# Performance work log

Measured on AMD Instinct MI355X. Metric: run time of the kernel, lower is better.

The kernel has to match this reference:

```python
import jax, jax.numpy as jnp
import numpy as np

B, N, H = 8, 128, 768      # batch, words, BERT hidden
HID, L = 384, 100          # MLP hidden, label_num


def setup_inputs() -> dict:
    key = jax.random.key(0)
    k0, k1, k2 = jax.random.split(key, 3)
    s = 0.02
    return {
        "repr_w": jax.random.normal(k0, (B, N, H), jnp.float32),
        "W1": jax.random.normal(k1, (2 * H, HID), jnp.float32) * s,
        "b1": jnp.zeros((HID,), jnp.float32),
        "W2": jax.random.normal(k2, (HID, L), jnp.float32) * s,
        "b2": jnp.zeros((L,), jnp.float32),
    }


def reference(repr_w, W1, b1, W2, b2):
    # Original: table[b,i,j] = concat(repr_w[b,j] (row_h), repr_w[b,i] (column_h))
    # then MLP: relu(table @ W1 + b1) @ W2 + b2  (dropout inactive in eval).
    # Decompose the concat-GEMM: concat(r_j, r_i) @ W1 == r_j @ W1[:H] + r_i @ W1[H:].
    W1_row, W1_col = W1[:H], W1[H:]
    p = jnp.einsum('bnh,hd->bnd', repr_w, W1_row)  # contribution indexed by j
    q = jnp.einsum('bnh,hd->bnd', repr_w, W1_col)  # contribution indexed by i
    h = jax.nn.relu(p[:, None, :, :] + q[:, :, None, :] + b1)  # [B,N,N,HID]
    return jnp.einsum('bijd,dl->bijl', h, W2) + b2              # [B,N,N,L]
```

## Files before the change

### kernel.cpp

```cpp
#include <hip/hip_runtime.h>
#include <hip/hip_bf16.h>

#define B_   8
#define N_   128
#define H_   768
#define HID_ 384
#define L_   100

typedef float f32x4 __attribute__((ext_vector_type(4)));
typedef short s16x8 __attribute__((ext_vector_type(8)));

__device__ __forceinline__ short f2bf(float f) {
    __hip_bfloat16 h = __float2bfloat16(f);
    return __builtin_bit_cast(short, h);
}

__device__ __forceinline__ void gl_lds16(const void* g, void* l) {
    __builtin_amdgcn_global_load_lds(
        (const __attribute__((address_space(1))) unsigned int*)g,
        (__attribute__((address_space(3))) unsigned int*)l, 16, 0, 0);
}

__global__ void prep_w1f(const float* __restrict__ W1, short* __restrict__ W1f) {
    int tid = blockIdx.x * 256 + threadIdx.x;
    if (tid >= 48 * 24 * 64) return;
    int lane = tid & 63;
    int kk   = (tid >> 6) % 24;
    int ct   = tid / (24 * 64);
    int c    = ct * 16 + (lane & 15);
    int k0   = kk * 32 + ((lane >> 4) << 3);
    short v[8];
#pragma unroll
    for (int e = 0; e < 8; ++e) {
        int k = k0 + e;
        float f = (c < HID_) ? W1[(size_t)k * HID_ + c]
                             : W1[(size_t)(H_ + k) * HID_ + (c - HID_)];
        v[e] = f2bf(f);
    }
    ((s16x8*)W1f)[tid] = *(const s16x8*)v;
}

__global__ void prep_w2f(const float* __restrict__ W2, short* __restrict__ W2f) {
    int tid = blockIdx.x * 256 + threadIdx.x;
    if (tid >= 12 * 7 * 64) return;
    int lane = tid & 63;
    int t    = (tid >> 6) % 7;
    int kk   = tid / (7 * 64);
    int c    = t * 16 + (lane & 15);
    int k0   = kk * 32 + ((lane >> 4) << 3);
    short v[8];
#pragma unroll
    for (int e = 0; e < 8; ++e) {
        float f = (c < L_) ? W2[(size_t)(k0 + e) * L_ + c] : 0.0f;
        v[e] = f2bf(f);
    }
    ((s16x8*)W2f)[tid] = *(const s16x8*)v;
}

__global__ __launch_bounds__(256) void pq_gemm(
    const float* __restrict__ repr, const short* __restrict__ W1f,
    const float* __restrict__ b1,
    float* __restrict__ Pt, float* __restrict__ Q)
{
    __shared__ float atile[192 * 16 * 4];
    const int rt   = blockIdx.x / 12;
    const int cg   = blockIdx.x % 12;
    const int w    = threadIdx.x >> 6;
    const int lane = threadIdx.x & 63;
    const int l15  = lane & 15;
    const int g    = lane >> 4;
    const int ct   = cg * 4 + w;
    const int row_g0 = rt * 16;

#pragma unroll
    for (int c = 0; c < 12; ++c) {
        int call = w * 12 + c;
        const float* src = repr + (size_t)(row_g0 + (lane & 15)) * H_
                         + (call * 4 + (lane >> 4)) * 4;
        gl_lds16(src, (char*)atile + call * 1024);
    }
    __syncthreads();

    f32x4 acc;
    acc[0] = 0.f; acc[1] = 0.f; acc[2] = 0.f; acc[3] = 0.f;
    const s16x8* bbase = (const s16x8*)W1f + (size_t)(ct * 24) * 64 + lane;

#pragma unroll 4
    for (int kk = 0; kk < 24; ++kk) {
        const int u0 = kk * 8 + g * 2;
        float a[8];
        *(float4*)&a[0] = *(const float4*)&atile[(u0 * 16 + l15) * 4];
        *(float4*)&a[4] = *(const float4*)&atile[((u0 + 1) * 16 + l15) * 4];
        s16x8 af;
#pragma unroll
        for (int e = 0; e < 8; ++e) af[e] = f2bf(a[e]);
        s16x8 bf = bbase[(size_t)kk * 64];
        acc = __builtin_amdgcn_mfma_f32_16x16x32_bf16(af, bf, acc, 0, 0, 0);
    }

    const int b = rt >> 3;
    const int c = ct * 16 + l15;
#pragma unroll
    for (int r = 0; r < 4; ++r) {
        int brow = (rt & 7) * 16 + g * 4 + r;
        float v = acc[r];
        if (c < HID_) {
            int slice = c >> 5, un = (c & 31) >> 2, e4 = c & 3;
            Pt[((((size_t)b * 12 + slice) * 8 + un) * 128 + brow) * 4 + e4] = v + b1[c];
        } else {
            Q[(size_t)(b * N_ + brow) * HID_ + (c - HID_)] = v;
        }
    }
}

__global__ __launch_bounds__(512, 4) void fused_out(
    const float* __restrict__ Pt, const float* __restrict__ Q,
    const short* __restrict__ W2f, const float* __restrict__ b2,
    float* __restrict__ out)
{
    __shared__ __align__(16) char smem[58368];
    char* pbufB  = smem;
    char* w2bufB = smem + 32768;
    char* qldsB  = smem + 47104;
    float* storeF = (float*)smem;

    const int blk  = blockIdx.x;
    const int b    = blk >> 6;
    const int i0   = (blk & 63) << 1;
    const int w    = threadIdx.x >> 6;
    const int lane = threadIdx.x & 63;
    const int l15  = lane & 15;
    const int g    = lane >> 4;

    const char* ptb = (const char*)Pt + (size_t)b * 12 * 16384;
    const char* w2g = (const char*)W2f;

    gl_lds16(ptb + w * 2048 + lane * 16,        pbufB + w * 2048);
    gl_lds16(ptb + w * 2048 + 1024 + lane * 16, pbufB + w * 2048 + 1024);
    if (w < 7)
        gl_lds16(w2g + w * 1024 + lane * 16, w2bufB + w * 1024);
    if (w == 7) {
        const char* qsrc = (const char*)(Q + (size_t)(b * N_ + i0) * HID_);
#pragma unroll
        for (int c2 = 0; c2 < 3; ++c2)
            gl_lds16(qsrc + c2 * 1024 + lane * 16, qldsB + c2 * 1024);
    }
    __syncthreads();

    f32x4 acc[2][7];
#pragma unroll
    for (int ii = 0; ii < 2; ++ii)
#pragma unroll
        for (int t = 0; t < 7; ++t) {
            acc[ii][t][0] = 0.f; acc[ii][t][1] = 0.f;
            acc[ii][t][2] = 0.f; acc[ii][t][3] = 0.f;
        }

    const float* qF = (const float*)qldsB;

#pragma unroll
    for (int kk = 0; kk < 12; ++kk) {
        const int cur = kk & 1;
        if (kk < 11) {
            const char* src = ptb + (size_t)(kk + 1) * 16384 + w * 2048;
            char* dst = pbufB + (cur ^ 1) * 16384 + w * 2048;
            gl_lds16(src + lane * 16,        dst);
            gl_lds16(src + 1024 + lane * 16, dst + 1024);
            if (w < 7)
                gl_lds16(w2g + (size_t)((kk + 1) * 7 + w) * 1024 + lane * 16,
                         w2bufB + (cur ^ 1) * 7168 + w * 1024);
        }

        const float* pF = (const float*)(pbufB + cur * 16384);
        float p[8], q0v[8], q1v[8];
        *(float4*)&p[0] = *(const float4*)&pF[((g * 2 + 0) * 128 + w * 16 + l15) * 4];
        *(float4*)&p[4] = *(const float4*)&pF[((g * 2 + 1) * 128 + w * 16 + l15) * 4];
        *(float4*)&q0v[0] = *(const float4*)&qF[0 * HID_ + kk * 32 + g * 8];
        *(float4*)&q0v[4] = *(const float4*)&qF[0 * HID_ + kk * 32 + g * 8 + 4];
        *(float4*)&q1v[0] = *(const float4*)&qF[1 * HID_ + kk * 32 + g * 8];
        *(float4*)&q1v[4] = *(const float4*)&qF[1 * HID_ + kk * 32 + g * 8 + 4];

        s16x8 af0, af1;
#pragma unroll
        for (int e = 0; e < 8; ++e) {
            af0[e] = f2bf(fmaxf(p[e] + q0v[e], 0.f));
            af1[e] = f2bf(fmaxf(p[e] + q1v[e], 0.f));
        }

        const s16x8* bfp = (const s16x8*)(w2bufB + cur * 7168) + lane;
#pragma unroll
        for (int t = 0; t < 7; ++t) {
            s16x8 bf = bfp[(size_t)t * 64];
            acc[0][t] = __builtin_amdgcn_mfma_f32_16x16x32_bf16(af0, bf, acc[0][t], 0, 0, 0);
            acc[1][t] = __builtin_amdgcn_mfma_f32_16x16x32_bf16(af1, bf, acc[1][t], 0, 0, 0);
        }
        __syncthreads();
    }

    float bias[7];
#pragma unroll
    for (int t = 0; t < 7; ++t) {
        int l = t * 16 + l15;
        bias[t] = (l < L_) ? b2[l] : 0.f;
    }

    __syncthreads();
    float* srow = storeF + w * (16 * 114);

#pragma unroll
    for (int ii = 0; ii < 2; ++ii) {
#pragma unroll
        for (int t = 0; t < 7; ++t)
#pragma unroll
            for (int r = 0; r < 4; ++r)
                srow[(g * 4 + r) * 114 + t * 16 + l15] = acc[ii][t][r] + bias[t];
        const size_t obase = (size_t)(b * N_ + (i0 + ii)) * N_ * L_;
#pragma unroll
        for (int row = 0; row < 16; ++row) {
            if (lane < 50) {
                float2 v = *(const float2*)&srow[row * 114 + lane * 2];
                *(float2*)(out + obase + (size_t)(w * 16 + row) * L_ + lane * 2) = v;
            }
        }
    }
}

extern "C" void kernel_launch(void* const* d_in, const int* in_sizes, int n_in,
                              void* d_out, int out_size, void* d_ws, size_t ws_size,
                              hipStream_t stream)
{
    const float* repr = (const float*)d_in[0];
    const float* W1   = (const float*)d_in[1];
    const float* b1   = (const float*)d_in[2];
    const float* W2   = (const float*)d_in[3];
    const float* b2   = (const float*)d_in[4];
    float* out = (float*)d_out;

    char* ws = (char*)d_ws;
    float* Pt  = (float*)(ws);
    float* Qm  = (float*)(ws + 1572864);
    short* W1f = (short*)(ws + 3145728);
    short* W2f = (short*)(ws + 4325376);

    hipLaunchKernelGGL(prep_w1f,  dim3(288), dim3(256), 0, stream, W1, W1f);
    hipLaunchKernelGGL(prep_w2f,  dim3(21),  dim3(256), 0, stream, W2, W2f);
    hipLaunchKernelGGL(pq_gemm,   dim3(768), dim3(256), 0, stream, repr, W1f, b1, Pt, Qm);
    hipLaunchKernelGGL(fused_out, dim3(512), dim3(512), 0, stream, Pt, Qm, W2f, b2, out);
}
```

Measured before the change: 108.1 us.

## Preload all of W2 into LDS, stream P from global, merge prep kernels

Merges the two weight-prep kernels into one launch to save a launch. In fused_out, all of W2f (84 KB) is staged into LDS once, and the per-step P tiles are register-prefetched straight from global memory. This removes the double-buffered LDS pipeline and the per-iteration __syncthreads. pq_gemm also gets a one-ahead register prefetch of the B fragments with full unroll. The cost is higher LDS use, which limits fused_out occupancy (launch bounds lowered to 2), and P is now read directly from global.

```diff
diff --git a/kernel.cpp b/kernel.cpp
--- a/kernel.cpp
+++ b/kernel.cpp
@@ -21,40 +21,39 @@
         (__attribute__((address_space(3))) unsigned int*)l, 16, 0, 0);
 }
 
-__global__ void prep_w1f(const float* __restrict__ W1, short* __restrict__ W1f) {
-    int tid = blockIdx.x * 256 + threadIdx.x;
-    if (tid >= 48 * 24 * 64) return;
-    int lane = tid & 63;
-    int kk   = (tid >> 6) % 24;
-    int ct   = tid / (24 * 64);
-    int c    = ct * 16 + (lane & 15);
-    int k0   = kk * 32 + ((lane >> 4) << 3);
-    short v[8];
-#pragma unroll
-    for (int e = 0; e < 8; ++e) {
-        int k = k0 + e;
-        float f = (c < HID_) ? W1[(size_t)k * HID_ + c]
-                             : W1[(size_t)(H_ + k) * HID_ + (c - HID_)];
-        v[e] = f2bf(f);
-    }
-    ((s16x8*)W1f)[tid] = *(const s16x8*)v;
-}
-
-__global__ void prep_w2f(const float* __restrict__ W2, short* __restrict__ W2f) {
-    int tid = blockIdx.x * 256 + threadIdx.x;
-    if (tid >= 12 * 7 * 64) return;
-    int lane = tid & 63;
-    int t    = (tid >> 6) % 7;
-    int kk   = tid / (7 * 64);
-    int c    = t * 16 + (lane & 15);
-    int k0   = kk * 32 + ((lane >> 4) << 3);
-    short v[8];
-#pragma unroll
-    for (int e = 0; e < 8; ++e) {
-        float f = (c < L_) ? W2[(size_t)(k0 + e) * L_ + c] : 0.0f;
-        v[e] = f2bf(f);
-    }
-    ((s16x8*)W2f)[tid] = *(const s16x8*)v;
+__global__ void prep_weights(const float* __restrict__ W1, const float* __restrict__ W2,
+                             short* __restrict__ W1f, short* __restrict__ W2f) {
+    if (blockIdx.x < 288) {
+        int tid  = blockIdx.x * 256 + threadIdx.x;
+        int lane = tid & 63;
+        int kk   = (tid >> 6) % 24;
+        int ct   = tid / (24 * 64);
+        int c    = ct * 16 + (lane & 15);
+        int k0   = kk * 32 + ((lane >> 4) << 3);
+        short v[8];
+#pragma unroll
+        for (int e = 0; e < 8; ++e) {
+            int k = k0 + e;
+            float f = (c < HID_) ? W1[(size_t)k * HID_ + c]
+                                 : W1[(size_t)(H_ + k) * HID_ + (c - HID_)];
+            v[e] = f2bf(f);
+        }
+        ((s16x8*)W1f)[tid] = *(const s16x8*)v;
+    } else {
+        int tid  = (blockIdx.x - 288) * 256 + threadIdx.x;
+        int lane = tid & 63;
+        int t    = (tid >> 6) % 7;
+        int kk   = tid / (7 * 64);
+        int c    = t * 16 + (lane & 15);
+        int k0   = kk * 32 + ((lane >> 4) << 3);
+        short v[8];
+#pragma unroll
+        for (int e = 0; e < 8; ++e) {
+            float f = (c < L_) ? W2[(size_t)(k0 + e) * L_ + c] : 0.0f;
+            v[e] = f2bf(f);
+        }
+        ((s16x8*)W2f)[tid] = *(const s16x8*)v;
+    }
 }
 
 __global__ __launch_bounds__(256) void pq_gemm(
@@ -85,8 +84,11 @@
     acc[0] = 0.f; acc[1] = 0.f; acc[2] = 0.f; acc[3] = 0.f;
     const s16x8* bbase = (const s16x8*)W1f + (size_t)(ct * 24) * 64 + lane;
 
-#pragma unroll 4
+    s16x8 lb = bbase[0];
+#pragma unroll
     for (int kk = 0; kk < 24; ++kk) {
+        s16x8 bf = lb;
+        if (kk < 23) lb = bbase[(size_t)(kk + 1) * 64];
         const int u0 = kk * 8 + g * 2;
         float a[8];
         *(float4*)&a[0] = *(const float4*)&atile[(u0 * 16 + l15) * 4];
@@ -94,7 +96,6 @@
         s16x8 af;
 #pragma unroll
         for (int e = 0; e < 8; ++e) af[e] = f2bf(a[e]);
-        s16x8 bf = bbase[(size_t)kk * 64];
         acc = __builtin_amdgcn_mfma_f32_16x16x32_bf16(af, bf, acc, 0, 0, 0);
     }
 
@@ -113,16 +114,15 @@
     }
 }
 
-__global__ __launch_bounds__(512, 4) void fused_out(
+__global__ __launch_bounds__(512, 2) void fused_out(
     const float* __restrict__ Pt, const float* __restrict__ Q,
     const short* __restrict__ W2f, const float* __restrict__ b2,
     float* __restrict__ out)
 {
-    __shared__ __align__(16) char smem[58368];
-    char* pbufB  = smem;
-    char* w2bufB = smem + 32768;
-    char* qldsB  = smem + 47104;
-    float* storeF = (float*)smem;
+    __shared__ __align__(16) char smem[89088];
+    const s16x8* w2s = (const s16x8*)smem;
+    const float* qF  = (const float*)(smem + 86016);
+    float* storeF    = (float*)smem;
 
     const int blk  = blockIdx.x;
     const int b    = blk >> 6;
@@ -132,18 +132,18 @@
     const int l15  = lane & 15;
     const int g    = lane >> 4;
 
-    const char* ptb = (const char*)Pt + (size_t)b * 12 * 16384;
-    const char* w2g = (const char*)W2f;
-
-    gl_lds16(ptb + w * 2048 + lane * 16,        pbufB + w * 2048);
-    gl_lds16(ptb + w * 2048 + 1024 + lane * 16, pbufB + w * 2048 + 1024);
-    if (w < 7)
-        gl_lds16(w2g + w * 1024 + lane * 16, w2bufB + w * 1024);
+#pragma unroll
+    for (int c = 0; c < 11; ++c) {
+        int call = w * 11 + c;
+        if (call < 84)
+            gl_lds16((const char*)W2f + call * 1024 + lane * 16,
+                     (char*)smem + call * 1024);
+    }
     if (w == 7) {
         const char* qsrc = (const char*)(Q + (size_t)(b * N_ + i0) * HID_);
 #pragma unroll
         for (int c2 = 0; c2 < 3; ++c2)
-            gl_lds16(qsrc + c2 * 1024 + lane * 16, qldsB + c2 * 1024);
+            gl_lds16(qsrc + c2 * 1024 + lane * 16, (char*)smem + 86016 + c2 * 1024);
     }
     __syncthreads();
 
@@ -156,25 +156,24 @@
             acc[ii][t][2] = 0.f; acc[ii][t][3] = 0.f;
         }
 
-    const float* qF = (const float*)qldsB;
+    const char* ptb = (const char*)Pt + (size_t)b * 12 * 16384;
+    const char* pt0 = ptb + (((g * 2 + 0) * 128) + w * 16 + l15) * 16;
+    const char* pt1 = ptb + (((g * 2 + 1) * 128) + w * 16 + l15) * 16;
+
+    float4 lp0 = *(const float4*)pt0;
+    float4 lp1 = *(const float4*)pt1;
 
 #pragma unroll
     for (int kk = 0; kk < 12; ++kk) {
-        const int cur = kk & 1;
+        float p[8];
+        *(float4*)&p[0] = lp0;
+        *(float4*)&p[4] = lp1;
         if (kk < 11) {
-            const char* src = ptb + (size_t)(kk + 1) * 16384 + w * 2048;
-            char* dst = pbufB + (cur ^ 1) * 16384 + w * 2048;
-            gl_lds16(src + lane * 16,        dst);
-            gl_lds16(src + 1024 + lane * 16, dst + 1024);
-            if (w < 7)
-                gl_lds16(w2g + (size_t)((kk + 1) * 7 + w) * 1024 + lane * 16,
-                         w2bufB + (cur ^ 1) * 7168 + w * 1024);
-        }
-
-        const float* pF = (const float*)(pbufB + cur * 16384);
-        float p[8], q0v[8], q1v[8];
-        *(float4*)&p[0] = *(const float4*)&pF[((g * 2 + 0) * 128 + w * 16 + l15) * 4];
-        *(float4*)&p[4] = *(const float4*)&pF[((g * 2 + 1) * 128 + w * 16 + l15) * 4];
+            lp0 = *(const float4*)(pt0 + (size_t)(kk + 1) * 16384);
+            lp1 = *(const float4*)(pt1 + (size_t)(kk + 1) * 16384);
+        }
+
+        float q0v[8], q1v[8];
         *(float4*)&q0v[0] = *(const float4*)&qF[0 * HID_ + kk * 32 + g * 8];
         *(float4*)&q0v[4] = *(const float4*)&qF[0 * HID_ + kk * 32 + g * 8 + 4];
         *(float4*)&q1v[0] = *(const float4*)&qF[1 * HID_ + kk * 32 + g * 8];
@@ -187,14 +186,13 @@
             af1[e] = f2bf(fmaxf(p[e] + q1v[e], 0.f));
         }
 
-        const s16x8* bfp = (const s16x8*)(w2bufB + cur * 7168) + lane;
+        const s16x8* bfp = w2s + (size_t)(kk * 7) * 64 + lane;
 #pragma unroll
         for (int t = 0; t < 7; ++t) {
             s16x8 bf = bfp[(size_t)t * 64];
             acc[0][t] = __builtin_amdgcn_mfma_f32_16x16x32_bf16(af0, bf, acc[0][t], 0, 0, 0);
             acc[1][t] = __builtin_amdgcn_mfma_f32_16x16x32_bf16(af1, bf, acc[1][t], 0, 0, 0);
         }
-        __syncthreads();
     }
 
     float bias[7];
@@ -242,8 +240,7 @@
     short* W1f = (short*)(ws + 3145728);
     short* W2f = (short*)(ws + 4325376);
 
-    hipLaunchKernelGGL(prep_w1f,  dim3(288), dim3(256), 0, stream, W1, W1f);
-    hipLaunchKernelGGL(prep_w2f,  dim3(21),  dim3(256), 0, stream, W2, W2f);
-    hipLaunchKernelGGL(pq_gemm,   dim3(768), dim3(256), 0, stream, repr, W1f, b1, Pt, Qm);
-    hipLaunchKernelGGL(fused_out, dim3(512), dim3(512), 0, stream, Pt, Qm, W2f, b2, out);
-}
+    hipLaunchKernelGGL(prep_weights, dim3(309), dim3(256), 0, stream, W1, W2, W1f, W2f);
+    hipLaunchKernelGGL(pq_gemm,      dim3(768), dim3(256), 0, stream, repr, W1f, b1, Pt, Qm);
+    hipLaunchKernelGGL(fused_out,    dim3(512), dim3(512), 0, stream, Pt, Qm, W2f, b2, out);
+}
```

New measurement: 109.0 us. No clear change (+0.8%).
